# Kernel optimization log

Hardware: AMD Instinct MI355X
Metric: run time of the kernel (lower is better)

Reference implementation:

```python
import jax, jax.numpy as jnp
import numpy as np

N = 50000   # nodes
E = 800000  # edges (avg degree 16)
D = 128     # emb_dim
K = 3       # message passing rounds


def setup_inputs() -> dict:
    key = jax.random.key(0)
    ks = jax.random.split(key, 24)
    scale = jnp.float32(0.1)  # keep k iterated MLP magnitudes sane

    def w(k, shape):
        return jax.random.normal(k, shape, dtype=jnp.float32) * scale

    inp = {
        "feat": jax.random.normal(ks[0], (N, D), dtype=jnp.float32),
        "src": jax.random.randint(ks[1], (E,), 0, N, dtype=jnp.int32),
        "dst": jax.random.randint(ks[2], (E,), 0, N, dtype=jnp.int32),
    }
    i = 3
    for name in ["nt", "fp", "fu", "bp", "bu"]:
        inp[name + "_w1"] = w(ks[i], (D, D))
        inp[name + "_b1"] = w(ks[i + 1], (D,))
        inp[name + "_w2"] = w(ks[i + 2], (D, D))
        inp[name + "_b2"] = w(ks[i + 3], (D,))
        i += 4
    return inp


def _fnn(x, w1, b1, w2, b2):
    # FNN(in,[hid],out): Linear -> ReLU -> Linear (no final activation)
    return jnp.maximum(x @ w1 + b1, 0.0) @ w2 + b2


def _aggregate(y, src, dst, pw1, pb1, pw2, pb2, uw1, ub1, uw2, ub2):
    # gather src node states -> edge MLP (+ReLU) -> scatter-sum -> node MLP (+ReLU)
    msg = jnp.maximum(_fnn(y[src], pw1, pb1, pw2, pb2), 0.0)   # [E, D]
    z = jax.ops.segment_sum(msg, dst, num_segments=N)          # [N, D]
    return jnp.maximum(_fnn(z, uw1, ub1, uw2, ub2), 0.0)       # [N, D]


def _message_pass(self_trans, src, dst, sink, params):
    y = self_trans
    for _ in range(K):
        h = _aggregate(y, src, dst, *params)
        h = h.at[sink].set(0.0)  # zero the sink node row
        y = self_trans + h
    return y


def reference(feat, src, dst,
              nt_w1, nt_b1, nt_w2, nt_b2,
              fp_w1, fp_b1, fp_w2, fp_b2,
              fu_w1, fu_b1, fu_w2, fu_b2,
              bp_w1, bp_b1, bp_w2, bp_b2,
              bu_w1, bu_b1, bu_w2, bu_b2):
    self_trans = _fnn(feat, nt_w1, nt_b1, nt_w2, nt_b2)  # [N, D]
    # forward-direction aggregator, sink = last node
    out_fpa = _message_pass(self_trans, src, dst, N - 1,
                            (fp_w1, fp_b1, fp_w2, fp_b2,
                             fu_w1, fu_b1, fu_w2, fu_b2))
    # reversed graph (dgl.reverse swaps src/dst), sink = node 0
    out_bpa = _message_pass(self_trans, dst, src, 0,
                            (bp_w1, bp_b1, bp_w2, bp_b2,
                             bu_w1, bu_b1, bu_w2, bu_b2))
    return jnp.concatenate([out_fpa, out_bpa], axis=1)  # [N, 2D]
```

## Files before the change

kernel.cpp:

```cpp
#include <hip/hip_runtime.h>

#define Nn 50000
#define Ee 800000
#define Dd 128
#define Kk 3
#define TE 64
#define TEA 32
#define NT 256

#define LSTR 136
#define WSLOT 32768

#define NBUK 196
#define SCH 2048
#define SB ((Ee + SCH - 1) / SCH)
#define FCAP 5632

typedef short sh8 __attribute__((ext_vector_type(8)));
typedef float f32x4 __attribute__((ext_vector_type(4)));

__device__ __forceinline__ ushort bfsplit(float x, float* rem) {
  const unsigned u = __float_as_uint(x);
  *rem = x - __uint_as_float(u & 0xffff0000u);
  return (ushort)(u >> 16);
}
__device__ __forceinline__ ushort bftrunc(float x) {
  return (ushort)(__float_as_uint(x) >> 16);
}
__device__ __forceinline__ ushort f32_to_bf16_rtn(float x) {
  const unsigned u = __float_as_uint(x);
  return (ushort)((u + 0x7fffu + ((u >> 16) & 1u)) >> 16);
}

__device__ __forceinline__ void acc8(const uint4 v, float4& a0, float4& a1) {
  a0.x += __uint_as_float(v.x << 16);
  a0.y += __uint_as_float(v.x & 0xffff0000u);
  a0.z += __uint_as_float(v.y << 16);
  a0.w += __uint_as_float(v.y & 0xffff0000u);
  a1.x += __uint_as_float(v.z << 16);
  a1.y += __uint_as_float(v.z & 0xffff0000u);
  a1.z += __uint_as_float(v.w << 16);
  a1.w += __uint_as_float(v.w & 0xffff0000u);
}

#define MFMA_LAYER(WH, WL, MT)                                                 \
  {                                                                            \
    _Pragma("unroll")                                                          \
    for (int c = 0; c < 4; ++c) {                                              \
      const sh8 bh0 = *(const sh8*)((WH) + (((nt0    ) * 4 + c) * 64 + lane) * 8); \
      const sh8 bh1 = *(const sh8*)((WH) + (((nt0 + 1) * 4 + c) * 64 + lane) * 8); \
      const sh8 bl0 = *(const sh8*)((WL) + (((nt0    ) * 4 + c) * 64 + lane) * 8); \
      const sh8 bl1 = *(const sh8*)((WL) + (((nt0 + 1) * 4 + c) * 64 + lane) * 8); \
      _Pragma("unroll")                                                        \
      for (int mt = 0; mt < (MT); ++mt) {                                      \
        const int aoff = (mt * 16 + l15) * LSTR + c * 32 + q8 * 8;             \
        const sh8 ah = *(const sh8*)(Sh + aoff);                               \
        const sh8 al = *(const sh8*)(Sl + aoff);                               \
        acc[mt][0] = __builtin_amdgcn_mfma_f32_16x16x32_bf16(ah, bh0, acc[mt][0], 0, 0, 0); \
        acc[mt][1] = __builtin_amdgcn_mfma_f32_16x16x32_bf16(ah, bh1, acc[mt][1], 0, 0, 0); \
        acc[mt][0] = __builtin_amdgcn_mfma_f32_16x16x32_bf16(al, bh0, acc[mt][0], 0, 0, 0); \
        acc[mt][1] = __builtin_amdgcn_mfma_f32_16x16x32_bf16(al, bh1, acc[mt][1], 0, 0, 0); \
        acc[mt][0] = __builtin_amdgcn_mfma_f32_16x16x32_bf16(ah, bl0, acc[mt][0], 0, 0, 0); \
        acc[mt][1] = __builtin_amdgcn_mfma_f32_16x16x32_bf16(ah, bl1, acc[mt][1], 0, 0, 0); \
      }                                                                        \
    }                                                                          \
  }

#define ZERO_ACC(MT)                                             \
  {                                                              \
    _Pragma("unroll")                                            \
    for (int mt = 0; mt < (MT); ++mt)                            \
      _Pragma("unroll")                                          \
      for (int nl = 0; nl < 2; ++nl) {                           \
        acc[mt][nl][0] = 0.f; acc[mt][nl][1] = 0.f;              \
        acc[mt][nl][2] = 0.f; acc[mt][nl][3] = 0.f;              \
      }                                                          \
  }

#define HIDDEN_TO_LDS(B1ptr, MT)                                 \
  {                                                              \
    const float b1a = (B1ptr)[w32 + l15];                        \
    const float b1b = (B1ptr)[w32 + 16 + l15];                   \
    _Pragma("unroll")                                            \
    for (int mt = 0; mt < (MT); ++mt)                            \
      _Pragma("unroll")                                          \
      for (int nl = 0; nl < 2; ++nl) {                           \
        const int col = w32 + nl * 16 + l15;                     \
        const float bb = nl ? b1b : b1a;                         \
        _Pragma("unroll")                                        \
        for (int rg = 0; rg < 4; ++rg) {                         \
          const int row = mt * 16 + q8 * 4 + rg;                 \
          const float h = fmaxf(acc[mt][nl][rg] + bb, 0.f);      \
          float rm;                                              \
          const ushort hh = bfsplit(h, &rm);                     \
          const int off = row * LSTR + col;                      \
          Sh[off] = hh;                                          \
          Sl[off] = bftrunc(rm);                                 \
        }                                                        \
      }                                                          \
  }

#define STC_TO_LDS(MT)                                           \
  {                                                              \
    _Pragma("unroll")                                            \
    for (int mt = 0; mt < (MT); ++mt)                            \
      _Pragma("unroll")                                          \
      for (int nl = 0; nl < 2; ++nl) {                           \
        const int col = w32 + nl * 16 + l15;                     \
        _Pragma("unroll")                                        \
        for (int rg = 0; rg < 4; ++rg) {                         \
          const int row = mt * 16 + q8 * 4 + rg;                 \
          float rm;                                              \
          const ushort hh = bfsplit(stc[mt][nl][rg], &rm);       \
          const int off = row * LSTR + col;                      \
          Sh[off] = hh;                                          \
          Sl[off] = bftrunc(rm);                                 \
        }                                                        \
      }                                                          \
  }

#define STAGE_ROWS(Xptr)                                                       \
  {                                                                            \
    _Pragma("unroll")                                                          \
    for (int it = 0; it < (TE * 32 / NT); ++it) {                              \
      const int i = t + NT * it;                                               \
      const int r = i >> 5;                                                    \
      const int c4 = (i & 31) << 2;                                            \
      float4 v = make_float4(0.f, 0.f, 0.f, 0.f);                              \
      if (r < nrow) v = *(const float4*)((Xptr) + (size_t)(row0 + r) * Dd + c4); \
      ushort4 hv, lv; float rm;                                                \
      hv.x = bfsplit(v.x, &rm); lv.x = bftrunc(rm);                            \
      hv.y = bfsplit(v.y, &rm); lv.y = bftrunc(rm);                            \
      hv.z = bfsplit(v.z, &rm); lv.z = bftrunc(rm);                            \
      hv.w = bfsplit(v.w, &rm); lv.w = bftrunc(rm);                            \
      *(ushort4*)(&Sh[r * LSTR + c4]) = hv;                                    \
      *(ushort4*)(&Sl[r * LSTR + c4]) = lv;                                    \
    }                                                                          \
  }

#define MFMA_PRELUDE(MT)                                         \
  const int lane = t & 63;                                       \
  const int wave = t >> 6;                                       \
  const int l15 = lane & 15;                                     \
  const int q8 = lane >> 4;                                      \
  const int w32 = wave * 32;                                     \
  const int nt0 = wave * 2;                                      \
  f32x4 acc[MT][2];

struct DirP {
  const ushort *u1, *u2, *p1, *p2;
  const float *ub1, *ub2, *pb1, *pb2;
};

__global__ __launch_bounds__(NT) void stmsg_kernel(
    const float* __restrict__ X,
    const ushort* __restrict__ Wn1, const ushort* __restrict__ Wn2,
    const float* __restrict__ Bn1, const float* __restrict__ Bn2,
    DirP pf, DirP pb,
    float* __restrict__ st, ushort* __restrict__ Mf, ushort* __restrict__ Mb)
{
  __shared__ __align__(16) ushort Sbuf[2 * TE * LSTR];
  ushort* Sh = Sbuf;
  ushort* Sl = Sbuf + TE * LSTR;
  const int t = threadIdx.x;
  const int row0 = blockIdx.x * TE;
  const int rem = Nn - row0;
  const int nrow = rem < TE ? rem : TE;

  STAGE_ROWS(X);
  __syncthreads();
  MFMA_PRELUDE(4);

  ZERO_ACC(4);
  MFMA_LAYER(Wn1, Wn1 + 16384, 4);
  __syncthreads();
  HIDDEN_TO_LDS(Bn1, 4);
  __syncthreads();
  ZERO_ACC(4);
  MFMA_LAYER(Wn2, Wn2 + 16384, 4);

  float stc[4][2][4];
  {
    const float b2a = Bn2[w32 + l15];
    const float b2b = Bn2[w32 + 16 + l15];
    #pragma unroll
    for (int mt = 0; mt < 4; ++mt)
      #pragma unroll
      for (int nl = 0; nl < 2; ++nl) {
        const int col = w32 + nl * 16 + l15;
        const float bb = nl ? b2b : b2a;
        #pragma unroll
        for (int rg = 0; rg < 4; ++rg) {
          const int row = mt * 16 + q8 * 4 + rg;
          const float v = acc[mt][nl][rg] + bb;
          stc[mt][nl][rg] = v;
          if (row < nrow) st[(size_t)(row0 + row) * Dd + col] = v;
        }
      }
  }
  __syncthreads();

  STC_TO_LDS(4);
  __syncthreads();
  ZERO_ACC(4);
  MFMA_LAYER(pf.p1, pf.p1 + 16384, 4);
  __syncthreads();
  HIDDEN_TO_LDS(pf.pb1, 4);
  __syncthreads();
  ZERO_ACC(4);
  MFMA_LAYER(pf.p2, pf.p2 + 16384, 4);
  {
    const float b2a = pf.pb2[w32 + l15];
    const float b2b = pf.pb2[w32 + 16 + l15];
    #pragma unroll
    for (int mt = 0; mt < 4; ++mt)
      #pragma unroll
      for (int nl = 0; nl < 2; ++nl) {
        const int col = w32 + nl * 16 + l15;
        const float bb = nl ? b2b : b2a;
        #pragma unroll
        for (int rg = 0; rg < 4; ++rg) {
          const int row = mt * 16 + q8 * 4 + rg;
          if (row < nrow)
            Mf[(size_t)(row0 + row) * Dd + col] =
                f32_to_bf16_rtn(fmaxf(acc[mt][nl][rg] + bb, 0.f));
        }
      }
  }
  __syncthreads();

  STC_TO_LDS(4);
  __syncthreads();
  ZERO_ACC(4);
  MFMA_LAYER(pb.p1, pb.p1 + 16384, 4);
  __syncthreads();
  HIDDEN_TO_LDS(pb.pb1, 4);
  __syncthreads();
  ZERO_ACC(4);
  MFMA_LAYER(pb.p2, pb.p2 + 16384, 4);
  {
    const float b2a = pb.pb2[w32 + l15];
    const float b2b = pb.pb2[w32 + 16 + l15];
    #pragma unroll
    for (int mt = 0; mt < 4; ++mt)
      #pragma unroll
      for (int nl = 0; nl < 2; ++nl) {
        const int col = w32 + nl * 16 + l15;
        const float bb = nl ? b2b : b2a;
        #pragma unroll
        for (int rg = 0; rg < 4; ++rg) {
          const int row = mt * 16 + q8 * 4 + rg;
          if (row < nrow)
            Mb[(size_t)(row0 + row) * Dd + col] =
                f32_to_bf16_rtn(fmaxf(acc[mt][nl][rg] + bb, 0.f));
        }
      }
  }
}

template <int DO_MSG>
__global__ __launch_bounds__(NT) void aggupdmsg_kernel(
    const ushort* __restrict__ Min_f, const ushort* __restrict__ Min_b,
    const int* __restrict__ rp_f, const int* __restrict__ rp_b,
    const int* __restrict__ col_f, const int* __restrict__ col_b,
    const float* __restrict__ st,
    ushort* __restrict__ RMf, ushort* __restrict__ RMb,
    float* __restrict__ RYf, float* __restrict__ RYb, int rstride,
    DirP pf, DirP pb, int nhalf)
{
  __shared__ __align__(16) ushort Sbuf[2 * TEA * LSTR];
  ushort* Sh = Sbuf;
  ushort* Sl = Sbuf + TEA * LSTR;
  const int t = threadIdx.x;
  const int dir = blockIdx.x >= nhalf;
  const int row0 = (blockIdx.x - dir * nhalf) * TEA;
  const int rem = Nn - row0;
  const int nrow = rem < TEA ? rem : TEA;
  const DirP P = dir ? pb : pf;
  const ushort* Min = dir ? Min_b : Min_f;
  const int* rp = dir ? rp_b : rp_f;
  const int* col = dir ? col_b : col_f;
  ushort* RoutM = dir ? RMb : RMf;
  float* RoutY = dir ? RYb : RYf;
  const int sink = dir ? 0 : (Nn - 1);

  {
    const int nr = t >> 3;
    const int o8 = t & 7;
    float4 za[4];
    #pragma unroll
    for (int i = 0; i < 4; ++i) za[i] = make_float4(0.f, 0.f, 0.f, 0.f);
    if (nr < nrow) {
      const int gnode = row0 + nr;
      int e = rp[gnode];
      const int ee = rp[gnode + 1];
      const ushort* Mo = Min + o8 * 16;
      for (; e + 3 < ee; e += 4) {
        const int c0 = col[e];
        const int c1 = col[e + 1];
        const int c2 = col[e + 2];
        const int c3 = col[e + 3];
        const ushort* r0 = Mo + (size_t)c0 * Dd;
        const ushort* r1 = Mo + (size_t)c1 * Dd;
        const ushort* r2 = Mo + (size_t)c2 * Dd;
        const ushort* r3 = Mo + (size_t)c3 * Dd;
        uint4 a0 = *(const uint4*)(r0), b0 = *(const uint4*)(r0 + 8);
        uint4 a1 = *(const uint4*)(r1), b1 = *(const uint4*)(r1 + 8);
        uint4 a2 = *(const uint4*)(r2), b2 = *(const uint4*)(r2 + 8);
        uint4 a3 = *(const uint4*)(r3), b3 = *(const uint4*)(r3 + 8);
        acc8(a0, za[0], za[1]); acc8(b0, za[2], za[3]);
        acc8(a1, za[0], za[1]); acc8(b1, za[2], za[3]);
        acc8(a2, za[0], za[1]); acc8(b2, za[2], za[3]);
        acc8(a3, za[0], za[1]); acc8(b3, za[2], za[3]);
      }
      for (; e < ee; ++e) {
        const ushort* r0 = Mo + (size_t)col[e] * Dd;
        acc8(*(const uint4*)(r0), za[0], za[1]);
        acc8(*(const uint4*)(r0 + 8), za[2], za[3]);
      }
    }
    #pragma unroll
    for (int k = 0; k < 4; ++k) {
      ushort4 hv, lv; float rm;
      hv.x = bfsplit(za[k].x, &rm); lv.x = bftrunc(rm);
      hv.y = bfsplit(za[k].y, &rm); lv.y = bftrunc(rm);
      hv.z = bfsplit(za[k].z, &rm); lv.z = bftrunc(rm);
      hv.w = bfsplit(za[k].w, &rm); lv.w = bftrunc(rm);
      const int c4 = o8 * 16 + k * 4;
      *(ushort4*)(&Sh[nr * LSTR + c4]) = hv;
      *(ushort4*)(&Sl[nr * LSTR + c4]) = lv;
    }
  }
  __syncthreads();

  MFMA_PRELUDE(2);

  ZERO_ACC(2);
  MFMA_LAYER(P.u1, P.u1 + 16384, 2);
  __syncthreads();
  HIDDEN_TO_LDS(P.ub1, 2);
  __syncthreads();
  ZERO_ACC(2);
  MFMA_LAYER(P.u2, P.u2 + 16384, 2);

  {
    const float b2a = P.ub2[w32 + l15];
    const float b2b = P.ub2[w32 + 16 + l15];
    if (DO_MSG) __syncthreads();
    #pragma unroll
    for (int mt = 0; mt < 2; ++mt)
      #pragma unroll
      for (int nl = 0; nl < 2; ++nl) {
        const int col = w32 + nl * 16 + l15;
        const float bb = nl ? b2b : b2a;
        #pragma unroll
        for (int rg = 0; rg < 4; ++rg) {
          const int row = mt * 16 + q8 * 4 + rg;
          float v = 0.f;
          if (row < nrow) {
            const int gr = row0 + row;
            v = fmaxf(acc[mt][nl][rg] + bb, 0.f);
            if (gr == sink) v = 0.f;
            v += st[(size_t)gr * Dd + col];
          }
          if (DO_MSG) {
            float rm;
            const ushort hh = bfsplit(v, &rm);
            const int off = row * LSTR + col;
            Sh[off] = hh;
            Sl[off] = bftrunc(rm);
          } else if (row < nrow) {
            RoutY[(size_t)(row0 + row) * rstride + col] = v;
          }
        }
      }
  }

  if (DO_MSG) {
    __syncthreads();
    ZERO_ACC(2);
    MFMA_LAYER(P.p1, P.p1 + 16384, 2);
    __syncthreads();
    HIDDEN_TO_LDS(P.pb1, 2);
    __syncthreads();
    ZERO_ACC(2);
    MFMA_LAYER(P.p2, P.p2 + 16384, 2);

    const float b2a = P.pb2[w32 + l15];
    const float b2b = P.pb2[w32 + 16 + l15];
    #pragma unroll
    for (int mt = 0; mt < 2; ++mt)
      #pragma unroll
      for (int nl = 0; nl < 2; ++nl) {
        const int col = w32 + nl * 16 + l15;
        const float bb = nl ? b2b : b2a;
        #pragma unroll
        for (int rg = 0; rg < 4; ++rg) {
          const int row = mt * 16 + q8 * 4 + rg;
          if (row < nrow)
            RoutM[(size_t)(row0 + row) * Dd + col] =
                f32_to_bf16_rtn(fmaxf(acc[mt][nl][rg] + bb, 0.f));
        }
      }
  }
}

struct WPtrs { const float* w[10]; };

__global__ void pack_w_kernel(WPtrs P, ushort* __restrict__ out)
{
  const int id = blockIdx.x * blockDim.x + threadIdx.x;
  const int mat = blockIdx.y;
  const int j = id & 7;
  const int lane = (id >> 3) & 63;
  const int ch = (id >> 9) & 3;
  const int nt = id >> 11;
  const int k = ch * 32 + (lane >> 4) * 8 + j;
  const int n = nt * 16 + (lane & 15);
  const float x = P.w[mat][k * Dd + n];
  float rm;
  const ushort h = bfsplit(x, &rm);
  out[(size_t)mat * WSLOT + id] = h;
  out[(size_t)mat * WSLOT + 16384 + id] = bftrunc(rm);
}

__global__ __launch_bounds__(256) void csr_count(
    const int* __restrict__ src, const int* __restrict__ dst,
    int* __restrict__ bcnt)
{
  const int dirv = blockIdx.y;
  const int* key = dirv ? src : dst;
  __shared__ int h[NBUK];
  const int t = threadIdx.x;
  if (t < NBUK) h[t] = 0;
  __syncthreads();
  const int e0 = blockIdx.x * SCH;
  #pragma unroll
  for (int i = 0; i < SCH / 256; ++i) {
    const int e = e0 + i * 256 + t;
    if (e < Ee) atomicAdd(&h[key[e] >> 8], 1);
  }
  __syncthreads();
  if (t < NBUK && h[t] > 0) atomicAdd(&bcnt[dirv * 256 + t], h[t]);
}

__global__ __launch_bounds__(256) void csr_scan(
    const int* __restrict__ bcnt, int* __restrict__ bbase,
    int* __restrict__ bcur, int* __restrict__ rp)
{
  __shared__ int s[256];
  const int t = threadIdx.x;
  for (int y = 0; y < 2; ++y) {
    const int v = (t < NBUK) ? bcnt[y * 256 + t] : 0;
    s[t] = v;
    __syncthreads();
    for (int off = 1; off < 256; off <<= 1) {
      int x = s[t];
      if (t >= off) x += s[t - off];
      __syncthreads();
      s[t] = x;
      __syncthreads();
    }
    const int excl = s[t] - v;
    if (t < NBUK) { bbase[y * 257 + t] = excl; bcur[y * 256 + t] = excl; }
    if (t == NBUK - 1) bbase[y * 257 + NBUK] = s[t];
    if (t == 0) rp[y * (Nn + 1) + Nn] = Ee;
    __syncthreads();
  }
}

__global__ __launch_bounds__(256) void csr_scatter(
    const int* __restrict__ src, const int* __restrict__ dst,
    int* __restrict__ bcur, uint* __restrict__ pairs)
{
  const int dirv = blockIdx.y;
  const int* key = dirv ? src : dst;
  const int* val = dirv ? dst : src;
  __shared__ int lh[NBUK], gb[NBUK], lc[NBUK];
  const int t = threadIdx.x;
  if (t < NBUK) { lh[t] = 0; lc[t] = 0; }
  __syncthreads();
  const int e0 = blockIdx.x * SCH;
  int ks[SCH / 256], vs[SCH / 256];
  #pragma unroll
  for (int i = 0; i < SCH / 256; ++i) {
    const int e = e0 + i * 256 + t;
    ks[i] = (e < Ee) ? key[e] : -1;
    vs[i] = (e < Ee) ? val[e] : 0;
    if (ks[i] >= 0) atomicAdd(&lh[ks[i] >> 8], 1);
  }
  __syncthreads();
  if (t < NBUK && lh[t] > 0) gb[t] = atomicAdd(&bcur[dirv * 256 + t], lh[t]);
  __syncthreads();
  uint* pd = pairs + (size_t)dirv * Ee;
  #pragma unroll
  for (int i = 0; i < SCH / 256; ++i) {
    if (ks[i] >= 0) {
      const int b = ks[i] >> 8;
      const int r = atomicAdd(&lc[b], 1);
      pd[gb[b] + r] = ((uint)ks[i] << 16) | (uint)vs[i];
    }
  }
}

__global__ __launch_bounds__(256) void csr_final(
    const uint* __restrict__ pairs, const int* __restrict__ bbase,
    int* __restrict__ rp, int* __restrict__ col_f, int* __restrict__ col_b)
{
  const int dirv = blockIdx.y;
  const int b = blockIdx.x;
  const int base = bbase[dirv * 257 + b];
  const int cnt = bbase[dirv * 257 + b + 1] - base;
  const uint* pd = pairs + (size_t)dirv * Ee + base;
  int* colo = dirv ? col_b : col_f;
  __shared__ int h[256];
  __shared__ int s[256];
  __shared__ uint pr[FCAP];
  __shared__ int cols[FCAP];
  const int t = threadIdx.x;
  h[t] = 0;
  __syncthreads();
  const bool fits = (cnt <= FCAP);
  if (fits) {
    for (int i = t; i < cnt; i += 256) {
      const uint p = pd[i];
      pr[i] = p;
      atomicAdd(&h[(p >> 16) & 255], 1);
    }
  } else {
    for (int i = t; i < cnt; i += 256) atomicAdd(&h[(pd[i] >> 16) & 255], 1);
  }
  __syncthreads();
  const int v = h[t];
  s[t] = v;
  __syncthreads();
  for (int off = 1; off < 256; off <<= 1) {
    int x = s[t];
    if (t >= off) x += s[t - off];
    __syncthreads();
    s[t] = x;
    __syncthreads();
  }
  const int excl = s[t] - v;
  const int node = b * 256 + t;
  if (node < Nn) rp[dirv * (Nn + 1) + node] = base + excl;
  h[t] = excl;
  __syncthreads();
  if (fits) {
    for (int band = 0; band < 8; ++band) {
      for (int i = t; i < cnt; i += 256) {
        const uint p = pr[i];
        const int vv = (int)(p & 0xffffu);
        if ((vv >> 13) == band) {
          const int k = (p >> 16) & 255;
          const int r = atomicAdd(&h[k], 1);
          cols[r] = vv;
        }
      }
      __syncthreads();
    }
    for (int i = t; i < cnt; i += 256) colo[base + i] = cols[i];
  } else {
    for (int i = t; i < cnt; i += 256) {
      const uint p = pd[i];
      const int k = (p >> 16) & 255;
      const int r = atomicAdd(&h[k], 1);
      colo[base + r] = (int)(p & 0xffffu);
    }
  }
}

extern "C" void kernel_launch(void* const* d_in, const int* in_sizes, int n_in,
                              void* d_out, int out_size, void* d_ws, size_t ws_size,
                              hipStream_t stream)
{
  const float* feat = (const float*)d_in[0];
  const int*   src  = (const int*)d_in[1];
  const int*   dst  = (const int*)d_in[2];

  const float* W[5][4];
  for (int p = 0; p < 5; ++p)
    for (int q = 0; q < 4; ++q)
      W[p][q] = (const float*)d_in[3 + p * 4 + q];

  float* st = (float*)d_ws;
  ushort* Mp_f = (ushort*)(st + (size_t)Nn * Dd);
  ushort* Mp_b = Mp_f + (size_t)Nn * Dd;
  ushort* Mq_f = Mp_b + (size_t)Nn * Dd;
  ushort* Mq_b = Mq_f + (size_t)Nn * Dd;
  int* ip       = (int*)(Mq_b + (size_t)Nn * Dd);
  int* rp_f     = ip;                 ip += Nn + 1;
  int* rp_b     = ip;                 ip += Nn + 1;
  int* col_f    = ip;                 ip += Ee;
  int* col_b    = ip;                 ip += Ee;
  int* bcnt     = ip;                 ip += 2 * 256;
  int* bbase    = ip;                 ip += 2 * 257;
  int* bcur     = ip;                 ip += 2 * 256;
  ushort* Wp = (ushort*)(((uintptr_t)ip + 63) & ~(uintptr_t)63);
  float* out = (float*)d_out;

  uint* pairs = (uint*)Mq_f;

  const int nodeBlocks = (Nn + TE - 1) / TE;
  const int aggBlocks  = (Nn + TEA - 1) / TEA;
  const int dualBlocks = 2 * aggBlocks;

  WPtrs wpk;
  for (int p = 0; p < 5; ++p) { wpk.w[2 * p] = W[p][0]; wpk.w[2 * p + 1] = W[p][2]; }
  pack_w_kernel<<<dim3(64, 10), NT, 0, stream>>>(wpk, Wp);

  hipMemsetAsync(bcnt, 0, 2 * 256 * sizeof(int), stream);
  csr_count<<<dim3(SB, 2), 256, 0, stream>>>(src, dst, bcnt);
  csr_scan<<<1, 256, 0, stream>>>(bcnt, bbase, bcur, rp_f);
  csr_scatter<<<dim3(SB, 2), 256, 0, stream>>>(src, dst, bcur, pairs);
  csr_final<<<dim3(NBUK, 2), 256, 0, stream>>>(pairs, bbase, rp_f, col_f, col_b);

  #define WS(m) (Wp + (size_t)(m) * WSLOT)
  DirP Pf = { WS(4), WS(5), WS(2), WS(3), W[2][1], W[2][3], W[1][1], W[1][3] };
  DirP Pb = { WS(8), WS(9), WS(6), WS(7), W[4][1], W[4][3], W[3][1], W[3][3] };

  stmsg_kernel<<<nodeBlocks, NT, 0, stream>>>(
      feat, WS(0), WS(1), W[0][1], W[0][3], Pf, Pb, st, Mp_f, Mp_b);

  aggupdmsg_kernel<1><<<dualBlocks, NT, 0, stream>>>(
      Mp_f, Mp_b, rp_f, rp_b, col_f, col_b, st,
      Mq_f, Mq_b, nullptr, nullptr, 0, Pf, Pb, aggBlocks);

  aggupdmsg_kernel<1><<<dualBlocks, NT, 0, stream>>>(
      Mq_f, Mq_b, rp_f, rp_b, col_f, col_b, st,
      Mp_f, Mp_b, nullptr, nullptr, 0, Pf, Pb, aggBlocks);

  aggupdmsg_kernel<0><<<dualBlocks, NT, 0, stream>>>(
      Mp_f, Mp_b, rp_f, rp_b, col_f, col_b, st,
      nullptr, nullptr, out, out + Dd, 2 * Dd, Pf, Pb, aggBlocks);

  #undef WS
}
```

Baseline: 544.9 us.

## Fuse weight packing into CSR scan, halve stmsg row tile, scatter columns directly

Weight packing moves into extra blocks of the CSR scan kernel, which removes one kernel launch. The stmsg kernel now handles 32 rows per block instead of 64, giving twice as many blocks and using less LDS and fewer registers. The per-bucket cols staging buffer in csr_final is dropped and columns are written straight to global memory. The trade-offs are more weight reloads per row in stmsg and scattered global writes in csr_final in place of coalesced ones.

```diff
diff --git a/kernel.cpp b/kernel.cpp
--- a/kernel.cpp
+++ b/kernel.cpp
@@ -4,7 +4,6 @@
 #define Ee 800000
 #define Dd 128
 #define Kk 3
-#define TE 64
 #define TEA 32
 #define NT 256
 
@@ -122,7 +121,7 @@
 #define STAGE_ROWS(Xptr)                                                       \
   {                                                                            \
     _Pragma("unroll")                                                          \
-    for (int it = 0; it < (TE * 32 / NT); ++it) {                              \
+    for (int it = 0; it < (TEA * 32 / NT); ++it) {                             \
       const int i = t + NT * it;                                               \
       const int r = i >> 5;                                                    \
       const int c4 = (i & 31) << 2;                                            \
@@ -159,32 +158,32 @@
     DirP pf, DirP pb,
     float* __restrict__ st, ushort* __restrict__ Mf, ushort* __restrict__ Mb)
 {
-  __shared__ __align__(16) ushort Sbuf[2 * TE * LSTR];
+  __shared__ __align__(16) ushort Sbuf[2 * TEA * LSTR];
   ushort* Sh = Sbuf;
-  ushort* Sl = Sbuf + TE * LSTR;
+  ushort* Sl = Sbuf + TEA * LSTR;
   const int t = threadIdx.x;
-  const int row0 = blockIdx.x * TE;
+  const int row0 = blockIdx.x * TEA;
   const int rem = Nn - row0;
-  const int nrow = rem < TE ? rem : TE;
+  const int nrow = rem < TEA ? rem : TEA;
 
   STAGE_ROWS(X);
   __syncthreads();
-  MFMA_PRELUDE(4);
-
-  ZERO_ACC(4);
-  MFMA_LAYER(Wn1, Wn1 + 16384, 4);
-  __syncthreads();
-  HIDDEN_TO_LDS(Bn1, 4);
-  __syncthreads();
-  ZERO_ACC(4);
-  MFMA_LAYER(Wn2, Wn2 + 16384, 4);
-
-  float stc[4][2][4];
+  MFMA_PRELUDE(2);
+
+  ZERO_ACC(2);
+  MFMA_LAYER(Wn1, Wn1 + 16384, 2);
+  __syncthreads();
+  HIDDEN_TO_LDS(Bn1, 2);
+  __syncthreads();
+  ZERO_ACC(2);
+  MFMA_LAYER(Wn2, Wn2 + 16384, 2);
+
+  float stc[2][2][4];
   {
     const float b2a = Bn2[w32 + l15];
     const float b2b = Bn2[w32 + 16 + l15];
     #pragma unroll
-    for (int mt = 0; mt < 4; ++mt)
+    for (int mt = 0; mt < 2; ++mt)
       #pragma unroll
       for (int nl = 0; nl < 2; ++nl) {
         const int col = w32 + nl * 16 + l15;
@@ -200,20 +199,20 @@
   }
   __syncthreads();
 
-  STC_TO_LDS(4);
-  __syncthreads();
-  ZERO_ACC(4);
-  MFMA_LAYER(pf.p1, pf.p1 + 16384, 4);
-  __syncthreads();
-  HIDDEN_TO_LDS(pf.pb1, 4);
-  __syncthreads();
-  ZERO_ACC(4);
-  MFMA_LAYER(pf.p2, pf.p2 + 16384, 4);
+  STC_TO_LDS(2);
+  __syncthreads();
+  ZERO_ACC(2);
+  MFMA_LAYER(pf.p1, pf.p1 + 16384, 2);
+  __syncthreads();
+  HIDDEN_TO_LDS(pf.pb1, 2);
+  __syncthreads();
+  ZERO_ACC(2);
+  MFMA_LAYER(pf.p2, pf.p2 + 16384, 2);
   {
     const float b2a = pf.pb2[w32 + l15];
     const float b2b = pf.pb2[w32 + 16 + l15];
     #pragma unroll
-    for (int mt = 0; mt < 4; ++mt)
+    for (int mt = 0; mt < 2; ++mt)
       #pragma unroll
       for (int nl = 0; nl < 2; ++nl) {
         const int col = w32 + nl * 16 + l15;
@@ -229,20 +228,20 @@
   }
   __syncthreads();
 
-  STC_TO_LDS(4);
-  __syncthreads();
-  ZERO_ACC(4);
-  MFMA_LAYER(pb.p1, pb.p1 + 16384, 4);
-  __syncthreads();
-  HIDDEN_TO_LDS(pb.pb1, 4);
-  __syncthreads();
-  ZERO_ACC(4);
-  MFMA_LAYER(pb.p2, pb.p2 + 16384, 4);
+  STC_TO_LDS(2);
+  __syncthreads();
+  ZERO_ACC(2);
+  MFMA_LAYER(pb.p1, pb.p1 + 16384, 2);
+  __syncthreads();
+  HIDDEN_TO_LDS(pb.pb1, 2);
+  __syncthreads();
+  ZERO_ACC(2);
+  MFMA_LAYER(pb.p2, pb.p2 + 16384, 2);
   {
     const float b2a = pb.pb2[w32 + l15];
     const float b2b = pb.pb2[w32 + 16 + l15];
     #pragma unroll
-    for (int mt = 0; mt < 4; ++mt)
+    for (int mt = 0; mt < 2; ++mt)
       #pragma unroll
       for (int nl = 0; nl < 2; ++nl) {
         const int col = w32 + nl * 16 + l15;
@@ -407,23 +406,6 @@
 
 struct WPtrs { const float* w[10]; };
 
-__global__ void pack_w_kernel(WPtrs P, ushort* __restrict__ out)
-{
-  const int id = blockIdx.x * blockDim.x + threadIdx.x;
-  const int mat = blockIdx.y;
-  const int j = id & 7;
-  const int lane = (id >> 3) & 63;
-  const int ch = (id >> 9) & 3;
-  const int nt = id >> 11;
-  const int k = ch * 32 + (lane >> 4) * 8 + j;
-  const int n = nt * 16 + (lane & 15);
-  const float x = P.w[mat][k * Dd + n];
-  float rm;
-  const ushort h = bfsplit(x, &rm);
-  out[(size_t)mat * WSLOT + id] = h;
-  out[(size_t)mat * WSLOT + 16384 + id] = bftrunc(rm);
-}
-
 __global__ __launch_bounds__(256) void csr_count(
     const int* __restrict__ src, const int* __restrict__ dst,
     int* __restrict__ bcnt)
@@ -444,28 +426,46 @@
   if (t < NBUK && h[t] > 0) atomicAdd(&bcnt[dirv * 256 + t], h[t]);
 }
 
-__global__ __launch_bounds__(256) void csr_scan(
+__global__ __launch_bounds__(256) void csr_scan_pack(
     const int* __restrict__ bcnt, int* __restrict__ bbase,
-    int* __restrict__ bcur, int* __restrict__ rp)
+    int* __restrict__ bcur, int* __restrict__ rp,
+    WPtrs P, ushort* __restrict__ out)
 {
-  __shared__ int s[256];
   const int t = threadIdx.x;
-  for (int y = 0; y < 2; ++y) {
-    const int v = (t < NBUK) ? bcnt[y * 256 + t] : 0;
-    s[t] = v;
-    __syncthreads();
-    for (int off = 1; off < 256; off <<= 1) {
-      int x = s[t];
-      if (t >= off) x += s[t - off];
+  if (blockIdx.x == 0) {
+    __shared__ int s[256];
+    for (int y = 0; y < 2; ++y) {
+      const int v = (t < NBUK) ? bcnt[y * 256 + t] : 0;
+      s[t] = v;
       __syncthreads();
-      s[t] = x;
+      for (int off = 1; off < 256; off <<= 1) {
+        int x = s[t];
+        if (t >= off) x += s[t - off];
+        __syncthreads();
+        s[t] = x;
+        __syncthreads();
+      }
+      const int excl = s[t] - v;
+      if (t < NBUK) { bbase[y * 257 + t] = excl; bcur[y * 256 + t] = excl; }
+      if (t == NBUK - 1) bbase[y * 257 + NBUK] = s[t];
+      if (t == 0) rp[y * (Nn + 1) + Nn] = Ee;
       __syncthreads();
     }
-    const int excl = s[t] - v;
-    if (t < NBUK) { bbase[y * 257 + t] = excl; bcur[y * 256 + t] = excl; }
-    if (t == NBUK - 1) bbase[y * 257 + NBUK] = s[t];
-    if (t == 0) rp[y * (Nn + 1) + Nn] = Ee;
-    __syncthreads();
+  } else {
+    const int work = (blockIdx.x - 1) * 256 + t;
+    const int mat = work >> 14;
+    const int id = work & 16383;
+    const int j = id & 7;
+    const int lane = (id >> 3) & 63;
+    const int ch = (id >> 9) & 3;
+    const int nt = id >> 11;
+    const int k = ch * 32 + (lane >> 4) * 8 + j;
+    const int n = nt * 16 + (lane & 15);
+    const float x = P.w[mat][k * Dd + n];
+    float rm;
+    const ushort h = bfsplit(x, &rm);
+    out[(size_t)mat * WSLOT + id] = h;
+    out[(size_t)mat * WSLOT + 16384 + id] = bftrunc(rm);
   }
 }
 
@@ -516,7 +516,6 @@
   __shared__ int h[256];
   __shared__ int s[256];
   __shared__ uint pr[FCAP];
-  __shared__ int cols[FCAP];
   const int t = threadIdx.x;
   h[t] = 0;
   __syncthreads();
@@ -554,12 +553,11 @@
         if ((vv >> 13) == band) {
           const int k = (p >> 16) & 255;
           const int r = atomicAdd(&h[k], 1);
-          cols[r] = vv;
+          colo[base + r] = vv;
         }
       }
       __syncthreads();
     }
-    for (int i = t; i < cnt; i += 256) colo[base + i] = cols[i];
   } else {
     for (int i = t; i < cnt; i += 256) {
       const uint p = pd[i];
@@ -601,17 +599,15 @@
 
   uint* pairs = (uint*)Mq_f;
 
-  const int nodeBlocks = (Nn + TE - 1) / TE;
   const int aggBlocks  = (Nn + TEA - 1) / TEA;
   const int dualBlocks = 2 * aggBlocks;
 
   WPtrs wpk;
   for (int p = 0; p < 5; ++p) { wpk.w[2 * p] = W[p][0]; wpk.w[2 * p + 1] = W[p][2]; }
-  pack_w_kernel<<<dim3(64, 10), NT, 0, stream>>>(wpk, Wp);
 
   hipMemsetAsync(bcnt, 0, 2 * 256 * sizeof(int), stream);
   csr_count<<<dim3(SB, 2), 256, 0, stream>>>(src, dst, bcnt);
-  csr_scan<<<1, 256, 0, stream>>>(bcnt, bbase, bcur, rp_f);
+  csr_scan_pack<<<641, 256, 0, stream>>>(bcnt, bbase, bcur, rp_f, wpk, Wp);
   csr_scatter<<<dim3(SB, 2), 256, 0, stream>>>(src, dst, bcur, pairs);
   csr_final<<<dim3(NBUK, 2), 256, 0, stream>>>(pairs, bbase, rp_f, col_f, col_b);
 
@@ -619,7 +615,7 @@
   DirP Pf = { WS(4), WS(5), WS(2), WS(3), W[2][1], W[2][3], W[1][1], W[1][3] };
   DirP Pb = { WS(8), WS(9), WS(6), WS(7), W[4][1], W[4][3], W[3][1], W[3][3] };
 
-  stmsg_kernel<<<nodeBlocks, NT, 0, stream>>>(
+  stmsg_kernel<<<aggBlocks, NT, 0, stream>>>(
       feat, WS(0), WS(1), W[0][1], W[0][3], Pf, Pb, st, Mp_f, Mp_b);
 
   aggupdmsg_kernel<1><<<dualBlocks, NT, 0, stream>>>(
```

After: 525.2 us. 3.6% less time.
